# Optimization experiments

Measured on AMD Instinct MI355X. Metric: run time of the kernel, lower is better.

## Reference

```python
import jax, jax.numpy as jnp
import numpy as np

DIM = 768
NUM_HEADS = 12
HEAD_DIM = DIM // NUM_HEADS
SCALE = HEAD_DIM ** -0.5


def setup_inputs() -> dict:
    key = jax.random.key(0)
    k1, k2, k3, k4 = jax.random.split(key, 4)
    x = jax.random.normal(k1, (4, 2048, DIM), dtype=jnp.float32)
    # Linear weights stored as [in, out] (torch stores [out, in]; math identical)
    w_qkv = jax.random.normal(k2, (DIM, 3 * DIM), dtype=jnp.float32) * (DIM ** -0.5)
    w_proj = jax.random.normal(k3, (DIM, DIM), dtype=jnp.float32) * (DIM ** -0.5)
    b_proj = jax.random.normal(k4, (DIM,), dtype=jnp.float32) * 0.02
    return {"x": x, "w_qkv": w_qkv, "w_proj": w_proj, "b_proj": b_proj}


def reference(x, w_qkv, w_proj, b_proj):
    b, n, d = x.shape
    qkv = x @ w_qkv  # [b, n, 3*d]
    # '(qkv h d)' layout: leading split is qkv, then heads, then head_dim
    qkv = qkv.reshape(b, n, 3, NUM_HEADS, HEAD_DIM).transpose(2, 0, 3, 1, 4)
    q, k, v = qkv[0], qkv[1], qkv[2]  # each [b, h, n, hd]
    alpha = jnp.einsum('bhqd,bhkd->bhqk', q, k) * SCALE  # [b, h, n, n]
    attn = jax.nn.softmax(alpha, axis=-1)
    out = jnp.einsum('bhqk,bhkd->bhqd', attn, v)  # [b, h, n, hd]
    out = out.transpose(0, 2, 1, 3).reshape(b, n, d)  # b n (h d)
    return out @ w_proj + b_proj
```

## Files before the change

### kernel.cpp

```cpp
#include <hip/hip_runtime.h>
#include <hip/hip_bf16.h>


typedef short s16x8 __attribute__((ext_vector_type(8)));
typedef short s16x4 __attribute__((ext_vector_type(4)));
typedef float f32x4 __attribute__((ext_vector_type(4)));
typedef float f32x16 __attribute__((ext_vector_type(16)));
typedef unsigned int u32;
typedef unsigned int u32x2 __attribute__((ext_vector_type(2)));
typedef unsigned int u32x4 __attribute__((ext_vector_type(4)));

#define NHEADS 12
#define HDIM   64
#define SEQ    2048
#define BATCH  4
#define DMODEL 768
#define MTOT   (BATCH*SEQ)
#define K3     (3*DMODEL)
#define QSCALE 0.18033688f

__device__ __forceinline__ short f2bf(float f) {
  return __builtin_bit_cast(short, __float2bfloat16(f));
}
__device__ __forceinline__ u32 pack2bf_rh(float lo, float hi) {
  u32 a = __builtin_bit_cast(u32, lo) + 0x8000u;
  u32 b = __builtin_bit_cast(u32, hi) + 0x8000u;
  return __builtin_amdgcn_perm(b, a, 0x07060302u);
}
__device__ __forceinline__ f32x4 mfma16(s16x8 a, s16x8 b, f32x4 c) {
  return __builtin_amdgcn_mfma_f32_16x16x32_bf16(a, b, c, 0, 0, 0);
}
__device__ __forceinline__ f32x16 mfma32(s16x8 a, s16x8 b, f32x16 c) {
  return __builtin_amdgcn_mfma_f32_32x32x16_bf16(a, b, c, 0, 0, 0);
}
__device__ __forceinline__ void gload_lds16(const void* g, void* l) {
  __builtin_amdgcn_global_load_lds(
      (const __attribute__((address_space(1))) void*)g,
      (__attribute__((address_space(3))) void*)l, 16, 0, 0);
}

__global__ __launch_bounds__(256) void k_cast4(const float* __restrict__ in,
                                               short* __restrict__ out, int n4) {
  int i = blockIdx.x * 256 + threadIdx.x;
  if (i < n4) {
    float4 f = reinterpret_cast<const float4*>(in)[i];
    s16x4 v;
    v[0] = f2bf(f.x); v[1] = f2bf(f.y); v[2] = f2bf(f.z); v[3] = f2bf(f.w);
    reinterpret_cast<s16x4*>(out)[i] = v;
  }
}

__global__ __launch_bounds__(256) void k_transpose_lds(const float* __restrict__ in,
                                                       short* __restrict__ out, int C) {
  __shared__ short t[64][74];
  const int tid = threadIdx.x;
  const int c0 = blockIdx.x * 64;
  const int r0 = blockIdx.y * 64;
  {
    const int r = tid >> 2, j0 = (tid & 3) * 16;
    const float* ip = in + (size_t)(r0 + r) * C + c0 + j0;
#pragma unroll
    for (int k = 0; k < 16; k += 4) {
      float4 f = *reinterpret_cast<const float4*>(ip + k);
      t[r][j0 + k + 0] = f2bf(f.x); t[r][j0 + k + 1] = f2bf(f.y);
      t[r][j0 + k + 2] = f2bf(f.z); t[r][j0 + k + 3] = f2bf(f.w);
    }
  }
  __syncthreads();
  {
    const int c = tid >> 2, rr0 = (tid & 3) * 16;
    short* op = out + (size_t)(c0 + c) * DMODEL + r0 + rr0;
#pragma unroll
    for (int k = 0; k < 16; k += 8) {
      s16x8 v;
#pragma unroll
      for (int q = 0; q < 8; ++q) v[q] = t[rr0 + k + q][c];
      *reinterpret_cast<s16x8*>(op + k) = v;
    }
  }
}

__global__ __launch_bounds__(256) void k_gemm_qkv(const short* __restrict__ Xb,
                                                  const short* __restrict__ WT,
                                                  short* __restrict__ Qb,
                                                  short* __restrict__ Kb,
                                                  short* __restrict__ Vt) {
  __shared__ short As[2][128 * 32];
  __shared__ short Bs[2][128 * 32];
  const int tid = threadIdx.x;
  const int orig = blockIdx.y * gridDim.x + blockIdx.x;
  const int wg = (orig & 7) * (1152 / 8) + (orig >> 3);
  const int n0 = (wg % 18) * 128, m0 = (wg / 18) * 128;
  const int lane = tid & 63, w = tid >> 6;
  const int wr = w >> 1, wc = w & 1;
  const int g = lane >> 4, r16 = lane & 15;

  const int srow = tid >> 2;
  const int sch  = (tid & 3) * 8;
  const short* ga1 = Xb + (size_t)(m0 + srow) * DMODEL + sch;
  const short* ga2 = Xb + (size_t)(m0 + srow + 64) * DMODEL + sch;
  const short* gb1 = WT + (size_t)(n0 + srow) * DMODEL + sch;
  const short* gb2 = WT + (size_t)(n0 + srow + 64) * DMODEL + sch;
  short* lA = &As[0][0] + w * 512;
  short* lB = &Bs[0][0] + w * 512;

#define GSTAGE(b, k0)                                                          \
  { gload_lds16(ga1 + (k0), lA + (b) * 4096);                                  \
    gload_lds16(ga2 + (k0), lA + (b) * 4096 + 2048);                           \
    gload_lds16(gb1 + (k0), lB + (b) * 4096);                                  \
    gload_lds16(gb2 + (k0), lB + (b) * 4096 + 2048); }

  f32x4 acc[4][4] = {};

  GSTAGE(0, 0)
  for (int t = 0; t < DMODEL / 32; ++t) {
    const int b = t & 1;
    if (t + 1 < DMODEL / 32) {
      GSTAGE(b ^ 1, (t + 1) * 32)
      asm volatile("s_waitcnt vmcnt(4)" ::: "memory");
    } else {
      asm volatile("s_waitcnt vmcnt(0)" ::: "memory");
    }
    __builtin_amdgcn_s_barrier();
    __builtin_amdgcn_sched_barrier(0);

    s16x8 a[4], bfr[4];
#pragma unroll
    for (int i = 0; i < 4; ++i)
      a[i] = *reinterpret_cast<const s16x8*>(&As[b][(wr * 64 + i * 16 + r16) * 32 + g * 8]);
#pragma unroll
    for (int j = 0; j < 4; ++j)
      bfr[j] = *reinterpret_cast<const s16x8*>(&Bs[b][(wc * 64 + j * 16 + r16) * 32 + g * 8]);
#pragma unroll
    for (int i = 0; i < 4; ++i)
#pragma unroll
      for (int j = 0; j < 4; ++j)
        acc[i][j] = mfma16(a[i], bfr[j], acc[i][j]);

    __builtin_amdgcn_sched_barrier(0);
    __builtin_amdgcn_s_barrier();
  }
#undef GSTAGE

#pragma unroll
  for (int i = 0; i < 4; ++i) {
#pragma unroll
    for (int jn = 0; jn < 4; ++jn) {
      const int c = n0 + wc * 64 + jn * 16 + r16;
#pragma unroll
      for (int rr = 0; rr < 4; ++rr) {
        const int m = m0 + wr * 64 + i * 16 + g * 4 + rr;
        const float a = acc[i][jn][rr];
        const int bb = m >> 11, ns = m & 2047;
        if (c < DMODEL) {
          const int h = c >> 6, d = c & 63;
          Qb[((bb * NHEADS + h) * SEQ + ns) * HDIM + d] = f2bf(a * QSCALE);
        } else if (c < 2 * DMODEL) {
          const int cc = c - DMODEL, h = cc >> 6, d = cc & 63;
          Kb[((bb * NHEADS + h) * SEQ + ns) * HDIM + d] = f2bf(a);
        } else {
          const int cc = c - 2 * DMODEL, h = cc >> 6, d = cc & 63;
          Vt[((bb * NHEADS + h) * HDIM + d) * SEQ + ns] = f2bf(a);
        }
      }
    }
  }
}

__global__ __launch_bounds__(256, 3) void k_attn(const short* __restrict__ Qb,
                                                 const short* __restrict__ Kb,
                                                 const short* __restrict__ Vtg,
                                                 short* __restrict__ Ctx) {
  __shared__ short Kt[2][64 * 64];
  __shared__ short Vt[2][64 * 64];

  const int tid = threadIdx.x, lane = tid & 63, w = tid >> 6;
  const int l31 = lane & 31, hi = lane >> 5;

  const int orig = blockIdx.y * gridDim.x + blockIdx.x;
  const int wg = (orig & 7) * (768 / 8) + (orig >> 3);
  const int qx = wg & 15;
  const int bh = wg >> 4;
  const int bb = bh / NHEADS, h = bh - bb * NHEADS;
  const int q0w = qx * 128 + w * 32;

  const short* Qp = Qb + (size_t)bh * SEQ * HDIM;
  const short* Kp = Kb + (size_t)bh * SEQ * HDIM;
  const short* Vp = Vtg + (size_t)bh * HDIM * SEQ;
  const int key4 = (lane & 7) << 4;

  const int sr1 = tid >> 3, sr2 = 32 + sr1;
  const int c1 = (tid & 7) ^ (sr1 & 7);
  const int c2 = (tid & 7) ^ (sr2 & 7);
  const short* kg1 = Kp + sr1 * HDIM + c1 * 8;
  const short* kg2 = Kp + sr2 * HDIM + c2 * 8;
  const short* vg1 = Vp + (size_t)sr1 * SEQ + c1 * 8;
  const short* vg2 = Vp + (size_t)sr2 * SEQ + c2 * 8;
  short* kld = &Kt[0][0] + w * 512;
  short* vld = &Vt[0][0] + w * 512;

#define STAGE(b, kb)                                                           \
  { gload_lds16(kg1 + (size_t)(kb) * HDIM, kld + (b) * 4096);                  \
    gload_lds16(kg2 + (size_t)(kb) * HDIM, kld + (b) * 4096 + 2048);           \
    gload_lds16(vg1 + (kb),                vld + (b) * 4096);                  \
    gload_lds16(vg2 + (kb),                vld + (b) * 4096 + 2048); }

  s16x8 aq[4];
#pragma unroll
  for (int kk = 0; kk < 4; ++kk)
    aq[kk] = *reinterpret_cast<const s16x8*>(&Qp[(q0w + l31) * HDIM + kk * 16 + hi * 8]);

  float mrun = -1e30f;
  float sacc = 0.f;
  f32x16 accO[2] = {};

  STAGE(0, 0)

  for (int t = 0; t < SEQ / 64; ++t) {
    const int b = t & 1;
    if (t + 1 < SEQ / 64) {
      STAGE(b ^ 1, (t + 1) * 64)
      asm volatile("s_waitcnt vmcnt(4)" ::: "memory");
    } else {
      asm volatile("s_waitcnt vmcnt(0)" ::: "memory");
    }
    __builtin_amdgcn_s_barrier();
    __builtin_amdgcn_sched_barrier(0);

    const char* Kc = (const char*)Kt[b];
    const char* Vc = (const char*)Vt[b];

    f32x16 s0 = {}, s1 = {};
    __builtin_amdgcn_s_setprio(1);
#pragma unroll
    for (int kk = 0; kk < 4; ++kk) {
      const int cb = kk * 32 + hi * 16;
      s16x8 k0_ = *(const s16x8*)(Kc + (((l31)      * 128 + cb) ^ key4));
      s16x8 k1_ = *(const s16x8*)(Kc + (((l31 + 32) * 128 + cb) ^ key4));
      s0 = mfma32(k0_, aq[kk], s0);
      s1 = mfma32(k1_, aq[kk], s1);
    }
    __builtin_amdgcn_s_setprio(0);

    float mx = s0[0];
#pragma unroll
    for (int r = 1; r < 16; ++r) mx = fmaxf(mx, s0[r]);
#pragma unroll
    for (int r = 0; r < 16; ++r) mx = fmaxf(mx, s1[r]);
    mx = fmaxf(mx, __shfl_xor(mx, 32));
    if (__any(mx > mrun + 8.f)) {
      float mnew = fmaxf(mrun, mx);
      float alpha = __builtin_amdgcn_exp2f(mrun - mnew);
      mrun = mnew;
#pragma unroll
      for (int r = 0; r < 16; ++r) { accO[0][r] *= alpha; accO[1][r] *= alpha; }
      sacc *= alpha;
    }

    u32 A0[8], A1[8];
    float rs = 0.f;
#pragma unroll
    for (int r2 = 0; r2 < 8; ++r2) {
      float pa = __builtin_amdgcn_exp2f(s0[2 * r2]     - mrun);
      float pb = __builtin_amdgcn_exp2f(s0[2 * r2 + 1] - mrun);
      rs += pa + pb;
      A0[r2] = pack2bf_rh(pa, pb);
      float pc = __builtin_amdgcn_exp2f(s1[2 * r2]     - mrun);
      float pd = __builtin_amdgcn_exp2f(s1[2 * r2 + 1] - mrun);
      rs += pc + pd;
      A1[r2] = pack2bf_rh(pc, pd);
    }
    sacc += rs;

    __builtin_amdgcn_s_setprio(1);
#define PVW(Akg, KGOFF, S)                                                     \
    { u32 F0 = Akg[4 * (S)],     F2 = Akg[4 * (S) + 2];                        \
      u32 F1 = Akg[4 * (S) + 1], F3 = Akg[4 * (S) + 3];                        \
      asm volatile("v_permlane32_swap_b32 %0, %1" : "+v"(F0), "+v"(F2));       \
      asm volatile("v_permlane32_swap_b32 %0, %1" : "+v"(F1), "+v"(F3));       \
      u32x4 uv; uv[0] = F0; uv[1] = F1; uv[2] = F2; uv[3] = F3;                \
      s16x8 pfrag = __builtin_bit_cast(s16x8, uv);                             \
      const int cb_ = (KGOFF) + (S) * 32 + hi * 16;                            \
      s16x8 v0_ = *(const s16x8*)(Vc + (((l31)      * 128 + cb_) ^ key4));     \
      s16x8 v1_ = *(const s16x8*)(Vc + (((l31 + 32) * 128 + cb_) ^ key4));     \
      accO[0] = mfma32(v0_, pfrag, accO[0]);                                   \
      accO[1] = mfma32(v1_, pfrag, accO[1]); }
    PVW(A0, 0, 0) PVW(A0, 0, 1) PVW(A1, 64, 0) PVW(A1, 64, 1)
#undef PVW
    __builtin_amdgcn_s_setprio(0);

    __builtin_amdgcn_sched_barrier(0);
    __builtin_amdgcn_s_barrier();
  }
#undef STAGE

  sacc += __shfl_xor(sacc, 32);
  const float inv = 1.0f / sacc;
  short* rowp = Ctx + (size_t)(bb * SEQ + q0w + l31) * DMODEL + h * HDIM + 4 * hi;
#pragma unroll
  for (int dt = 0; dt < 2; ++dt) {
#pragma unroll
    for (int rq = 0; rq < 4; ++rq) {
      u32x2 ov;
      ov[0] = pack2bf_rh(accO[dt][rq * 4 + 0] * inv, accO[dt][rq * 4 + 1] * inv);
      ov[1] = pack2bf_rh(accO[dt][rq * 4 + 2] * inv, accO[dt][rq * 4 + 3] * inv);
      *reinterpret_cast<u32x2*>(rowp + dt * 32 + rq * 8) = ov;
    }
  }
}

__global__ __launch_bounds__(256) void k_gemm_proj(const short* __restrict__ Ctx,
                                                   const short* __restrict__ WT,
                                                   const float* __restrict__ bias,
                                                   float* __restrict__ Out) {
  __shared__ short As[2][128 * 32];
  __shared__ short Bs[2][128 * 32];
  const int tid = threadIdx.x;
  const int orig = blockIdx.y * gridDim.x + blockIdx.x;
  const int wg = (orig & 7) * (384 / 8) + (orig >> 3);
  const int n0 = (wg % 6) * 128, m0 = (wg / 6) * 128;
  const int lane = tid & 63, w = tid >> 6;
  const int wr = w >> 1, wc = w & 1;
  const int g = lane >> 4, r16 = lane & 15;

  const int srow = tid >> 2;
  const int sch  = (tid & 3) * 8;
  const short* ga1 = Ctx + (size_t)(m0 + srow) * DMODEL + sch;
  const short* ga2 = Ctx + (size_t)(m0 + srow + 64) * DMODEL + sch;
  const short* gb1 = WT + (size_t)(n0 + srow) * DMODEL + sch;
  const short* gb2 = WT + (size_t)(n0 + srow + 64) * DMODEL + sch;
  short* lA = &As[0][0] + w * 512;
  short* lB = &Bs[0][0] + w * 512;

#define GSTAGE(b, k0)                                                          \
  { gload_lds16(ga1 + (k0), lA + (b) * 4096);                                  \
    gload_lds16(ga2 + (k0), lA + (b) * 4096 + 2048);                           \
    gload_lds16(gb1 + (k0), lB + (b) * 4096);                                  \
    gload_lds16(gb2 + (k0), lB + (b) * 4096 + 2048); }

  f32x4 acc[4][4] = {};

  GSTAGE(0, 0)
  for (int t = 0; t < DMODEL / 32; ++t) {
    const int b = t & 1;
    if (t + 1 < DMODEL / 32) {
      GSTAGE(b ^ 1, (t + 1) * 32)
      asm volatile("s_waitcnt vmcnt(4)" ::: "memory");
    } else {
      asm volatile("s_waitcnt vmcnt(0)" ::: "memory");
    }
    __builtin_amdgcn_s_barrier();
    __builtin_amdgcn_sched_barrier(0);

    s16x8 a[4], bfr[4];
#pragma unroll
    for (int i = 0; i < 4; ++i)
      a[i] = *reinterpret_cast<const s16x8*>(&As[b][(wr * 64 + i * 16 + r16) * 32 + g * 8]);
#pragma unroll
    for (int j = 0; j < 4; ++j)
      bfr[j] = *reinterpret_cast<const s16x8*>(&Bs[b][(wc * 64 + j * 16 + r16) * 32 + g * 8]);
#pragma unroll
    for (int i = 0; i < 4; ++i)
#pragma unroll
      for (int j = 0; j < 4; ++j)
        acc[i][j] = mfma16(a[i], bfr[j], acc[i][j]);

    __builtin_amdgcn_sched_barrier(0);
    __builtin_amdgcn_s_barrier();
  }
#undef GSTAGE

#pragma unroll
  for (int i = 0; i < 4; ++i) {
#pragma unroll
    for (int jn = 0; jn < 4; ++jn) {
      const int c = n0 + wc * 64 + jn * 16 + r16;
      const float bv = bias[c];
#pragma unroll
      for (int rr = 0; rr < 4; ++rr) {
        const int m = m0 + wr * 64 + i * 16 + g * 4 + rr;
        Out[(size_t)m * DMODEL + c] = acc[i][jn][rr] + bv;
      }
    }
  }
}

extern "C" void kernel_launch(void* const* d_in, const int* in_sizes, int n_in,
                              void* d_out, int out_size, void* d_ws, size_t ws_size,
                              hipStream_t stream) {
  const float* x      = (const float*)d_in[0];
  const float* w_qkv  = (const float*)d_in[1];
  const float* w_proj = (const float*)d_in[2];
  const float* b_proj = (const float*)d_in[3];
  float* out = (float*)d_out;

  char* ws = (char*)d_ws;
  const size_t SZ_X = (size_t)MTOT * DMODEL * 2;
  short* Xb     = (short*)ws;                 ws += SZ_X;
  short* WqkvT  = (short*)ws;                 ws += (size_t)K3 * DMODEL * 2;
  short* WprojT = (short*)ws;                 ws += (size_t)DMODEL * DMODEL * 2;
  short* Qb     = (short*)ws;                 ws += SZ_X;
  short* Kb     = (short*)ws;                 ws += SZ_X;
  short* Vt     = (short*)ws;                 ws += SZ_X;
  short* Ctxb   = Xb;

  k_cast4<<<(MTOT * DMODEL / 4) / 256, 256, 0, stream>>>(x, Xb, MTOT * DMODEL / 4);
  k_transpose_lds<<<dim3(K3 / 64, DMODEL / 64), 256, 0, stream>>>(w_qkv, WqkvT, K3);
  k_transpose_lds<<<dim3(DMODEL / 64, DMODEL / 64), 256, 0, stream>>>(w_proj, WprojT, DMODEL);

  k_gemm_qkv<<<dim3(K3 / 128, MTOT / 128), 256, 0, stream>>>(Xb, WqkvT, Qb, Kb, Vt);
  k_attn<<<dim3(SEQ / 128, BATCH * NHEADS), 256, 0, stream>>>(Qb, Kb, Vt, Ctxb);
  k_gemm_proj<<<dim3(DMODEL / 128, MTOT / 128), 256, 0, stream>>>(Ctxb, WprojT, b_proj, out);
}
```

Baseline: 185.8 us.

## Double GEMM K-tile to 64 with XOR-swizzled LDS layout

Both the QKV and projection GEMMs now stage 64-wide K slices instead of 32, halving the number of loop iterations and barrier pairs per tile. Global-to-LDS loads use an XOR swizzle on the 16-byte chunk index so the fragment reads avoid bank conflicts at the new 128-byte row stride. This doubles LDS use per block, which may lower occupancy, and it deepens the vmcnt wait window.

```diff
diff --git a/kernel.cpp b/kernel.cpp
--- a/kernel.cpp
+++ b/kernel.cpp
@@ -85,8 +85,8 @@
                                                   short* __restrict__ Qb,
                                                   short* __restrict__ Kb,
                                                   short* __restrict__ Vt) {
-  __shared__ short As[2][128 * 32];
-  __shared__ short Bs[2][128 * 32];
+  __shared__ short As[2][128 * 64];
+  __shared__ short Bs[2][128 * 64];
   const int tid = threadIdx.x;
   const int orig = blockIdx.y * gridDim.x + blockIdx.x;
   const int wg = (orig & 7) * (1152 / 8) + (orig >> 3);
@@ -95,47 +95,57 @@
   const int wr = w >> 1, wc = w & 1;
   const int g = lane >> 4, r16 = lane & 15;
 
-  const int srow = tid >> 2;
-  const int sch  = (tid & 3) * 8;
-  const short* ga1 = Xb + (size_t)(m0 + srow) * DMODEL + sch;
-  const short* ga2 = Xb + (size_t)(m0 + srow + 64) * DMODEL + sch;
-  const short* gb1 = WT + (size_t)(n0 + srow) * DMODEL + sch;
-  const short* gb2 = WT + (size_t)(n0 + srow + 64) * DMODEL + sch;
+  const int srow = tid >> 3;
+  const int scc  = (tid & 7) ^ (srow & 7);
+  const short* gaA = Xb + (size_t)(m0 + srow) * DMODEL + scc * 8;
+  const short* gaB = WT + (size_t)(n0 + srow) * DMODEL + scc * 8;
   short* lA = &As[0][0] + w * 512;
   short* lB = &Bs[0][0] + w * 512;
 
 #define GSTAGE(b, k0)                                                          \
-  { gload_lds16(ga1 + (k0), lA + (b) * 4096);                                  \
-    gload_lds16(ga2 + (k0), lA + (b) * 4096 + 2048);                           \
-    gload_lds16(gb1 + (k0), lB + (b) * 4096);                                  \
-    gload_lds16(gb2 + (k0), lB + (b) * 4096 + 2048); }
+  { _Pragma("unroll")                                                          \
+    for (int L = 0; L < 4; ++L) {                                              \
+      gload_lds16(gaA + (size_t)(L * 32) * DMODEL + (k0),                      \
+                  lA + (b) * 8192 + L * 2048);                                 \
+      gload_lds16(gaB + (size_t)(L * 32) * DMODEL + (k0),                      \
+                  lB + (b) * 8192 + L * 2048);                                 \
+    } }
 
   f32x4 acc[4][4] = {};
+  const int key = (r16 & 7) << 4;
 
   GSTAGE(0, 0)
-  for (int t = 0; t < DMODEL / 32; ++t) {
+  for (int t = 0; t < DMODEL / 64; ++t) {
     const int b = t & 1;
-    if (t + 1 < DMODEL / 32) {
-      GSTAGE(b ^ 1, (t + 1) * 32)
-      asm volatile("s_waitcnt vmcnt(4)" ::: "memory");
+    if (t + 1 < DMODEL / 64) {
+      GSTAGE(b ^ 1, (t + 1) * 64)
+      asm volatile("s_waitcnt vmcnt(8)" ::: "memory");
     } else {
       asm volatile("s_waitcnt vmcnt(0)" ::: "memory");
     }
     __builtin_amdgcn_s_barrier();
     __builtin_amdgcn_sched_barrier(0);
 
-    s16x8 a[4], bfr[4];
+    const char* Ab = (const char*)&As[0][0] + b * 16384;
+    const char* Bb = (const char*)&Bs[0][0] + b * 16384;
+    s16x8 a[4][2], bf[4][2];
 #pragma unroll
     for (int i = 0; i < 4; ++i)
-      a[i] = *reinterpret_cast<const s16x8*>(&As[b][(wr * 64 + i * 16 + r16) * 32 + g * 8]);
+#pragma unroll
+      for (int kk = 0; kk < 2; ++kk)
+        a[i][kk] = *(const s16x8*)(Ab + (((wr * 64 + i * 16 + r16) * 128 + kk * 64 + g * 16) ^ key));
 #pragma unroll
     for (int j = 0; j < 4; ++j)
-      bfr[j] = *reinterpret_cast<const s16x8*>(&Bs[b][(wc * 64 + j * 16 + r16) * 32 + g * 8]);
-#pragma unroll
-    for (int i = 0; i < 4; ++i)
-#pragma unroll
-      for (int j = 0; j < 4; ++j)
-        acc[i][j] = mfma16(a[i], bfr[j], acc[i][j]);
+#pragma unroll
+      for (int kk = 0; kk < 2; ++kk)
+        bf[j][kk] = *(const s16x8*)(Bb + (((wc * 64 + j * 16 + r16) * 128 + kk * 64 + g * 16) ^ key));
+#pragma unroll
+    for (int kk = 0; kk < 2; ++kk)
+#pragma unroll
+      for (int i = 0; i < 4; ++i)
+#pragma unroll
+        for (int j = 0; j < 4; ++j)
+          acc[i][j] = mfma16(a[i][kk], bf[j][kk], acc[i][j]);
 
     __builtin_amdgcn_sched_barrier(0);
     __builtin_amdgcn_s_barrier();
@@ -313,8 +323,8 @@
                                                    const short* __restrict__ WT,
                                                    const float* __restrict__ bias,
                                                    float* __restrict__ Out) {
-  __shared__ short As[2][128 * 32];
-  __shared__ short Bs[2][128 * 32];
+  __shared__ short As[2][128 * 64];
+  __shared__ short Bs[2][128 * 64];
   const int tid = threadIdx.x;
   const int orig = blockIdx.y * gridDim.x + blockIdx.x;
   const int wg = (orig & 7) * (384 / 8) + (orig >> 3);
@@ -323,47 +333,57 @@
   const int wr = w >> 1, wc = w & 1;
   const int g = lane >> 4, r16 = lane & 15;
 
-  const int srow = tid >> 2;
-  const int sch  = (tid & 3) * 8;
-  const short* ga1 = Ctx + (size_t)(m0 + srow) * DMODEL + sch;
-  const short* ga2 = Ctx + (size_t)(m0 + srow + 64) * DMODEL + sch;
-  const short* gb1 = WT + (size_t)(n0 + srow) * DMODEL + sch;
-  const short* gb2 = WT + (size_t)(n0 + srow + 64) * DMODEL + sch;
+  const int srow = tid >> 3;
+  const int scc  = (tid & 7) ^ (srow & 7);
+  const short* gaA = Ctx + (size_t)(m0 + srow) * DMODEL + scc * 8;
+  const short* gaB = WT + (size_t)(n0 + srow) * DMODEL + scc * 8;
   short* lA = &As[0][0] + w * 512;
   short* lB = &Bs[0][0] + w * 512;
 
 #define GSTAGE(b, k0)                                                          \
-  { gload_lds16(ga1 + (k0), lA + (b) * 4096);                                  \
-    gload_lds16(ga2 + (k0), lA + (b) * 4096 + 2048);                           \
-    gload_lds16(gb1 + (k0), lB + (b) * 4096);                                  \
-    gload_lds16(gb2 + (k0), lB + (b) * 4096 + 2048); }
+  { _Pragma("unroll")                                                          \
+    for (int L = 0; L < 4; ++L) {                                              \
+      gload_lds16(gaA + (size_t)(L * 32) * DMODEL + (k0),                      \
+                  lA + (b) * 8192 + L * 2048);                                 \
+      gload_lds16(gaB + (size_t)(L * 32) * DMODEL + (k0),                      \
+                  lB + (b) * 8192 + L * 2048);                                 \
+    } }
 
   f32x4 acc[4][4] = {};
+  const int key = (r16 & 7) << 4;
 
   GSTAGE(0, 0)
-  for (int t = 0; t < DMODEL / 32; ++t) {
+  for (int t = 0; t < DMODEL / 64; ++t) {
     const int b = t & 1;
-    if (t + 1 < DMODEL / 32) {
-      GSTAGE(b ^ 1, (t + 1) * 32)
-      asm volatile("s_waitcnt vmcnt(4)" ::: "memory");
+    if (t + 1 < DMODEL / 64) {
+      GSTAGE(b ^ 1, (t + 1) * 64)
+      asm volatile("s_waitcnt vmcnt(8)" ::: "memory");
     } else {
       asm volatile("s_waitcnt vmcnt(0)" ::: "memory");
     }
     __builtin_amdgcn_s_barrier();
     __builtin_amdgcn_sched_barrier(0);
 
-    s16x8 a[4], bfr[4];
+    const char* Ab = (const char*)&As[0][0] + b * 16384;
+    const char* Bb = (const char*)&Bs[0][0] + b * 16384;
+    s16x8 a[4][2], bf[4][2];
 #pragma unroll
     for (int i = 0; i < 4; ++i)
-      a[i] = *reinterpret_cast<const s16x8*>(&As[b][(wr * 64 + i * 16 + r16) * 32 + g * 8]);
+#pragma unroll
+      for (int kk = 0; kk < 2; ++kk)
+        a[i][kk] = *(const s16x8*)(Ab + (((wr * 64 + i * 16 + r16) * 128 + kk * 64 + g * 16) ^ key));
 #pragma unroll
     for (int j = 0; j < 4; ++j)
-      bfr[j] = *reinterpret_cast<const s16x8*>(&Bs[b][(wc * 64 + j * 16 + r16) * 32 + g * 8]);
-#pragma unroll
-    for (int i = 0; i < 4; ++i)
-#pragma unroll
-      for (int j = 0; j < 4; ++j)
-        acc[i][j] = mfma16(a[i], bfr[j], acc[i][j]);
+#pragma unroll
+      for (int kk = 0; kk < 2; ++kk)
+        bf[j][kk] = *(const s16x8*)(Bb + (((wc * 64 + j * 16 + r16) * 128 + kk * 64 + g * 16) ^ key));
+#pragma unroll
+    for (int kk = 0; kk < 2; ++kk)
+#pragma unroll
+      for (int i = 0; i < 4; ++i)
+#pragma unroll
+        for (int j = 0; j < 4; ++j)
+          acc[i][j] = mfma16(a[i][kk], bf[j][kk], acc[i][j]);
 
     __builtin_amdgcn_sched_barrier(0);
     __builtin_amdgcn_s_barrier();
```

Result: faster. 170.6 us (-8.2%).
